# Kernel optimization log

Hardware: AMD Instinct MI355X
Metric: run time of the kernel (lower is better)

Reference implementation:

```python
import jax, jax.numpy as jnp
import numpy as np

TOP_K = 5
THRESHOLD = 0.0
EPS = 1e-12

def l2_normalize(x, axis):
    sq = jnp.sum(x * x, axis=axis, keepdims=True)
    return x * jax.lax.rsqrt(jnp.maximum(sq, EPS))

def setup_inputs() -> dict:
    key = jax.random.key(0)
    k1, k2, k3, k4 = jax.random.split(key, 4)
    B, S, D = 256, 197, 768
    P, L, T = 20, 5, 10
    x_embed = jax.random.normal(k1, (B, S, D), dtype=jnp.float32)
    prompt = jax.random.uniform(k2, (P, L, D), dtype=jnp.float32, minval=-1.0, maxval=1.0)
    prompt_key = jax.random.uniform(k3, (P, D), dtype=jnp.float32, minval=-1.0, maxval=1.0)
    assist_prompt = jax.random.uniform(k4, (T, L, D), dtype=jnp.float32, minval=-1.0, maxval=1.0)
    return {"x_embed": x_embed, "prompt": prompt, "prompt_key": prompt_key,
            "assist_prompt": assist_prompt, "test": 0}

def reference(x_embed, prompt, prompt_key, assist_prompt, test):
    B = x_embed.shape[0]
    D = x_embed.shape[-1]
    # embedding key: mean over tokens
    x_mean = jnp.mean(x_embed, axis=1)                 # [B, D]
    x_norm = l2_normalize(x_mean, axis=1)              # [B, D]  (test >= 0 branch)
    p_norm = l2_normalize(prompt_key, axis=1)          # [P, D]
    similarity = x_norm @ p_norm.T                     # [B, P]
    vals, idx = jax.lax.top_k(similarity, TOP_K)       # sorted descending -> pruning mask is a prefix
    keep = vals > THRESHOLD                            # [B, K]
    idx_pruned = jnp.where(keep, idx, -1)              # [B, K], -1 = dummy prompt
    idx_safe = jnp.maximum(idx_pruned, 0)
    # gather selected prompts, zero-out pruned slots (dummy prompts)
    sel = jnp.where(keep[:, :, None, None], prompt[idx_safe], 0.0)     # [B, K, L, D]
    assist_b = jnp.broadcast_to(assist_prompt, (B,) + assist_prompt.shape)  # [B, T, L, D]
    selected = jnp.concatenate([assist_b, sel], axis=1)                # [B, T+K, L, D]
    tokens = selected.reshape(B, -1, D)                                # [B, (T+K)*L, D]
    # reduce_sim: sum over all valid (b,k) keys of key . x_b', summed over b', / B
    gathered_keys = jnp.where(keep[:, :, None], p_norm[idx_safe], 0.0) # [B, K, D]
    key_total = jnp.sum(gathered_keys, axis=(0, 1))                    # [D]
    reduce_sim = jnp.dot(jnp.sum(x_norm, axis=0), key_total) / B
    prompted_embedding = jnp.concatenate([tokens, x_embed], axis=1)    # [B, (T+K)*L + S, D]
    return prompted_embedding, reduce_sim, tokens, idx_pruned, x_norm
```

## Files before the change

kernel.cpp:

```cpp
#include <hip/hip_runtime.h>

#define B 256
#define S 197
#define D 768
#define P 20
#define L 5
#define T 10
#define K 5

#define ROWS_PE 272
#define SZ_PE   (B * ROWS_PE * D)
#define OFF_RS  ((long)SZ_PE)
#define OFF_TOK (OFF_RS + 1)
#define SZ_TOK  (B * (T + K) * L * D)
#define OFF_IDX (OFF_TOK + SZ_TOK)
#define OFF_XN  (OFF_IDX + B * K)

typedef float f4 __attribute__((ext_vector_type(4)));

__global__ void __launch_bounds__(192)
k_mean_copy(const float* __restrict__ x, float* __restrict__ pe,
            float* __restrict__ partial) {
    const int tile = blockIdx.x & 3;
    const int b = blockIdx.x >> 2;
    const int t = threadIdx.x;
    const int s0 = tile * 50;
    const int s1 = (s0 + 50 < S) ? s0 + 50 : S;
    const f4* x4 = (const f4*)x;
    f4* o4 = (f4*)pe;
    const int xbase = b * S * (D / 4) + t;
    const int obase = (b * ROWS_PE + (T + K) * L) * (D / 4) + t;
    f4 acc = {0.f, 0.f, 0.f, 0.f};
    for (int s = s0; s < s1; ++s) {
        f4 v = __builtin_nontemporal_load(x4 + xbase + s * (D / 4));
        acc += v;
        __builtin_nontemporal_store(v, o4 + obase + s * (D / 4));
    }
    ((f4*)partial)[blockIdx.x * (D / 4) + t] = acc;
}

__global__ void __launch_bounds__(256)
k_fuse(const float* __restrict__ partial, const float* __restrict__ pkey,
       const float* __restrict__ prompt, const float* __restrict__ assist,
       float* __restrict__ pe, float* __restrict__ tok,
       float* __restrict__ xnorm_out, float* __restrict__ idxp_f,
       float* __restrict__ xsum, int* __restrict__ keycnt,
       unsigned int* __restrict__ done, float* __restrict__ rs) {
    const int t = threadIdx.x;

    if (blockIdx.x >= B) {
        const int item = (blockIdx.x - B) * 256 + t;
        const int b = item / 9600;
        const int r = item - b * 9600;
        const int j = r / 192;
        const int c = r - j * 192;
        const f4 v = ((const f4*)assist)[j * 192 + c];
        __builtin_nontemporal_store(v, (f4*)pe + ((long)b * ROWS_PE + j) * 192 + c);
        float* d2 = tok + ((long)b * 75 + j) * 768 + 4 * c;
        __builtin_nontemporal_store(v[0], d2 + 0);
        __builtin_nontemporal_store(v[1], d2 + 1);
        __builtin_nontemporal_store(v[2], d2 + 2);
        __builtin_nontemporal_store(v[3], d2 + 3);
        return;
    }

    const int b = blockIdx.x;
    const int lane = t & 63, wid = t >> 6;
    __shared__ float xs[D];
    __shared__ float sim[P];
    __shared__ float red[4];
    __shared__ float coef[P];
    __shared__ int sidx[K];
    __shared__ int amLast;

    float v0 = 0.f, v1 = 0.f, v2 = 0.f;
    for (int tile = 0; tile < 4; ++tile) {
        const float* pp = partial + (b * 4 + tile) * D;
        v0 += pp[t]; v1 += pp[t + 256]; v2 += pp[t + 512];
    }
    const float invS = 1.0f / (float)S;
    v0 *= invS; v1 *= invS; v2 *= invS;
    float ss = v0 * v0 + v1 * v1 + v2 * v2;
    for (int o = 32; o > 0; o >>= 1) ss += __shfl_down(ss, o);
    if (lane == 0) red[wid] = ss;
    __syncthreads();
    if (t == 0) red[0] = rsqrtf(fmaxf(red[0] + red[1] + red[2] + red[3], 1e-12f));
    __syncthreads();
    const float rn = red[0];
    v0 *= rn; v1 *= rn; v2 *= rn;
    xs[t] = v0; xs[t + 256] = v1; xs[t + 512] = v2;
    xnorm_out[b * D + t] = v0;
    xnorm_out[b * D + t + 256] = v1;
    xnorm_out[b * D + t + 512] = v2;
    atomicAdd(&xsum[t], v0);
    atomicAdd(&xsum[t + 256], v1);
    atomicAdd(&xsum[t + 512], v2);
    __syncthreads();

    for (int p = wid; p < P; p += 4) {
        const float* pr = pkey + p * D;
        float axk = 0.f, akk = 0.f;
        for (int d = lane; d < D; d += 64) {
            const float kv = pr[d];
            axk += xs[d] * kv;
            akk += kv * kv;
        }
        for (int o = 32; o > 0; o >>= 1) {
            axk += __shfl_down(axk, o);
            akk += __shfl_down(akk, o);
        }
        if (lane == 0) sim[p] = axk * rsqrtf(fmaxf(akk, 1e-12f));
    }
    __syncthreads();

    if (t == 0) {
        unsigned usedMask = 0u;
        for (int k = 0; k < K; ++k) {
            float best = -INFINITY; int bi = 0;
            for (int p = 0; p < P; ++p)
                if (!((usedMask >> p) & 1u) && sim[p] > best) { best = sim[p]; bi = p; }
            usedMask |= 1u << bi;
            const int oi = (best > 0.0f) ? bi : -1;
            sidx[k] = oi;
            idxp_f[b * K + k] = (float)oi;
            if (oi >= 0) atomicAdd(&keycnt[bi], 1);
        }
    }
    __syncthreads();

    for (int it = t; it < K * L * 192; it += 256) {
        const int j = it / 192;
        const int c = it - j * 192;
        const int k = j / L;
        const int l = j - k * L;
        const int idx = sidx[k];
        f4 v = {0.f, 0.f, 0.f, 0.f};
        if (idx >= 0) v = ((const f4*)prompt)[(idx * L + l) * 192 + c];
        __builtin_nontemporal_store(v, (f4*)pe + ((long)b * ROWS_PE + T * L + j) * 192 + c);
        float* d2 = tok + ((long)b * 75 + T * L + j) * 768 + 4 * c;
        __builtin_nontemporal_store(v[0], d2 + 0);
        __builtin_nontemporal_store(v[1], d2 + 1);
        __builtin_nontemporal_store(v[2], d2 + 2);
        __builtin_nontemporal_store(v[3], d2 + 3);
    }

    if (t == 0) {
        __threadfence();
        const unsigned prev =
            __hip_atomic_fetch_add(done, 1u, __ATOMIC_ACQ_REL, __HIP_MEMORY_SCOPE_AGENT);
        amLast = (prev == (unsigned)(B - 1)) ? 1 : 0;
    }
    __syncthreads();
    if (amLast) {
        for (int p = wid; p < P; p += 4) {
            const float* pr = pkey + p * D;
            float akk = 0.f;
            for (int d = lane; d < D; d += 64) { const float kv = pr[d]; akk += kv * kv; }
            for (int o = 32; o > 0; o >>= 1) akk += __shfl_down(akk, o);
            if (lane == 0) {
                const int cnt =
                    __hip_atomic_load(&keycnt[p], __ATOMIC_RELAXED, __HIP_MEMORY_SCOPE_AGENT);
                coef[p] = (float)cnt * rsqrtf(fmaxf(akk, 1e-12f));
            }
        }
        __syncthreads();
        float acc = 0.f;
        for (int cc = 0; cc < 3; ++cc) {
            const int d = t + cc * 256;
            float kt = 0.f;
            for (int p = 0; p < P; ++p) kt += coef[p] * pkey[p * D + d];
            const float xv =
                __hip_atomic_load(&xsum[d], __ATOMIC_RELAXED, __HIP_MEMORY_SCOPE_AGENT);
            acc += xv * kt;
        }
        for (int o = 32; o > 0; o >>= 1) acc += __shfl_down(acc, o);
        if (lane == 0) red[wid] = acc;
        __syncthreads();
        if (t == 0) rs[0] = (red[0] + red[1] + red[2] + red[3]) * (1.0f / (float)B);
    }
}

extern "C" void kernel_launch(void* const* d_in, const int* in_sizes, int n_in,
                              void* d_out, int out_size, void* d_ws, size_t ws_size,
                              hipStream_t stream) {
    const float* x      = (const float*)d_in[0];
    const float* prompt = (const float*)d_in[1];
    const float* pkey   = (const float*)d_in[2];
    const float* assist = (const float*)d_in[3];
    float* out = (float*)d_out;
    float* ws  = (float*)d_ws;

    float* partial   = ws;
    int*   keycnt    = (int*)(partial + B * 4 * D);
    float* xsum      = (float*)(keycnt + P);
    unsigned* done   = (unsigned*)(xsum + D);

    hipMemsetAsync(keycnt, 0, (P + D + 1) * sizeof(float), stream);

    k_mean_copy<<<dim3(4 * B), 192, 0, stream>>>(x, out, partial);
    k_fuse<<<dim3(B + 9600), 256, 0, stream>>>(partial, pkey, prompt, assist,
                                               out, out + OFF_TOK,
                                               out + OFF_XN, out + OFF_IDX,
                                               xsum, keycnt, done, out + OFF_RS);
}
```

Baseline: 449.8 us.

## Fuse mean-copy and per-batch fuse kernels via last-tile-arrives election

Merges the two kernels into one launch. Each of the four sequence tiles per batch row atomically increments a per-row counter after writing its partial sum, and the last tile to arrive does the normalize, similarity, top-k and prompt gather for that row. The goal is to drop one kernel launch and the grid-wide barrier between the streaming copy and the per-row work, so the gathers can overlap with ongoing copying. In exchange, the copy blocks now run with 256 threads while only 192 do work, and it adds atomic counter traffic.

```diff
diff --git a/kernel.cpp b/kernel.cpp
--- a/kernel.cpp
+++ b/kernel.cpp
@@ -16,40 +16,24 @@
 #define OFF_IDX (OFF_TOK + SZ_TOK)
 #define OFF_XN  (OFF_IDX + B * K)
 
+#define NPROD   (4 * B)
+#define NASSIST 9600
+
 typedef float f4 __attribute__((ext_vector_type(4)));
 
-__global__ void __launch_bounds__(192)
-k_mean_copy(const float* __restrict__ x, float* __restrict__ pe,
-            float* __restrict__ partial) {
-    const int tile = blockIdx.x & 3;
-    const int b = blockIdx.x >> 2;
+__global__ void __launch_bounds__(256)
+k_all(const float* __restrict__ x, const float* __restrict__ prompt,
+      const float* __restrict__ pkey, const float* __restrict__ assist,
+      float* __restrict__ pe, float* __restrict__ tok,
+      float* __restrict__ xnorm_out, float* __restrict__ idxp_f,
+      float* __restrict__ partial, float* __restrict__ xsum,
+      int* __restrict__ keycnt, unsigned* __restrict__ tile_done,
+      unsigned* __restrict__ done, float* __restrict__ rs) {
     const int t = threadIdx.x;
-    const int s0 = tile * 50;
-    const int s1 = (s0 + 50 < S) ? s0 + 50 : S;
-    const f4* x4 = (const f4*)x;
-    f4* o4 = (f4*)pe;
-    const int xbase = b * S * (D / 4) + t;
-    const int obase = (b * ROWS_PE + (T + K) * L) * (D / 4) + t;
-    f4 acc = {0.f, 0.f, 0.f, 0.f};
-    for (int s = s0; s < s1; ++s) {
-        f4 v = __builtin_nontemporal_load(x4 + xbase + s * (D / 4));
-        acc += v;
-        __builtin_nontemporal_store(v, o4 + obase + s * (D / 4));
-    }
-    ((f4*)partial)[blockIdx.x * (D / 4) + t] = acc;
-}
-
-__global__ void __launch_bounds__(256)
-k_fuse(const float* __restrict__ partial, const float* __restrict__ pkey,
-       const float* __restrict__ prompt, const float* __restrict__ assist,
-       float* __restrict__ pe, float* __restrict__ tok,
-       float* __restrict__ xnorm_out, float* __restrict__ idxp_f,
-       float* __restrict__ xsum, int* __restrict__ keycnt,
-       unsigned int* __restrict__ done, float* __restrict__ rs) {
-    const int t = threadIdx.x;
-
-    if (blockIdx.x >= B) {
-        const int item = (blockIdx.x - B) * 256 + t;
+    const int blk = blockIdx.x;
+
+    if (blk >= NPROD) {
+        const int item = (blk - NPROD) * 256 + t;
         const int b = item / 9600;
         const int r = item - b * 9600;
         const int j = r / 192;
@@ -64,7 +48,35 @@
         return;
     }
 
-    const int b = blockIdx.x;
+    const int b = blk >> 2;
+    const int tile = blk & 3;
+    if (t < 192) {
+        const int s0 = tile * 50;
+        const int s1 = (s0 + 50 < S) ? s0 + 50 : S;
+        const f4* x4 = (const f4*)x;
+        f4* o4 = (f4*)pe;
+        const int xbase = b * S * 192 + t;
+        const int obase = (b * ROWS_PE + (T + K) * L) * 192 + t;
+        f4 acc = {0.f, 0.f, 0.f, 0.f};
+        for (int s = s0; s < s1; ++s) {
+            f4 v = __builtin_nontemporal_load(x4 + xbase + s * 192);
+            acc += v;
+            __builtin_nontemporal_store(v, o4 + obase + s * 192);
+        }
+        ((f4*)partial)[blk * 192 + t] = acc;
+    }
+
+    __shared__ int winner;
+    __syncthreads();
+    if (t == 0) {
+        __threadfence();
+        const unsigned prev = __hip_atomic_fetch_add(
+            &tile_done[b], 1u, __ATOMIC_ACQ_REL, __HIP_MEMORY_SCOPE_AGENT);
+        winner = (prev == 3u) ? 1 : 0;
+    }
+    __syncthreads();
+    if (!winner) return;
+
     const int lane = t & 63, wid = t >> 6;
     __shared__ float xs[D];
     __shared__ float sim[P];
@@ -74,9 +86,11 @@
     __shared__ int amLast;
 
     float v0 = 0.f, v1 = 0.f, v2 = 0.f;
-    for (int tile = 0; tile < 4; ++tile) {
-        const float* pp = partial + (b * 4 + tile) * D;
-        v0 += pp[t]; v1 += pp[t + 256]; v2 += pp[t + 512];
+    for (int tl = 0; tl < 4; ++tl) {
+        float* pp = partial + (b * 4 + tl) * D;
+        v0 += __hip_atomic_load(pp + t,       __ATOMIC_RELAXED, __HIP_MEMORY_SCOPE_AGENT);
+        v1 += __hip_atomic_load(pp + t + 256, __ATOMIC_RELAXED, __HIP_MEMORY_SCOPE_AGENT);
+        v2 += __hip_atomic_load(pp + t + 512, __ATOMIC_RELAXED, __HIP_MEMORY_SCOPE_AGENT);
     }
     const float invS = 1.0f / (float)S;
     v0 *= invS; v1 *= invS; v2 *= invS;
@@ -190,16 +204,15 @@
     float* out = (float*)d_out;
     float* ws  = (float*)d_ws;
 
-    float* partial   = ws;
-    int*   keycnt    = (int*)(partial + B * 4 * D);
-    float* xsum      = (float*)(keycnt + P);
-    unsigned* done   = (unsigned*)(xsum + D);
-
-    hipMemsetAsync(keycnt, 0, (P + D + 1) * sizeof(float), stream);
-
-    k_mean_copy<<<dim3(4 * B), 192, 0, stream>>>(x, out, partial);
-    k_fuse<<<dim3(B + 9600), 256, 0, stream>>>(partial, pkey, prompt, assist,
-                                               out, out + OFF_TOK,
-                                               out + OFF_XN, out + OFF_IDX,
-                                               xsum, keycnt, done, out + OFF_RS);
+    float*    partial   = ws;
+    int*      keycnt    = (int*)(partial + 4 * B * D);
+    float*    xsum      = (float*)(keycnt + P);
+    unsigned* done      = (unsigned*)(xsum + D);
+    unsigned* tile_done = done + 1;
+
+    hipMemsetAsync(keycnt, 0, (P + D + 1 + B) * sizeof(float), stream);
+
+    k_all<<<dim3(NPROD + NASSIST), 256, 0, stream>>>(
+        x, prompt, pkey, assist, out, out + OFF_TOK, out + OFF_XN, out + OFF_IDX,
+        partial, xsum, keycnt, tile_done, done, out + OFF_RS);
 }
```

Result: slower. 514.5 us (+14.4%).

## Fold memset into stream kernel, double threads per tile, vectorize token stores

Applied to the files above, without the earlier changes.

Removes the separate hipMemsetAsync by adding an extra block to the streaming kernel that zeroes the counters. The streaming kernel now uses 384 threads, with two halves interleaving rows and combining partial sums through LDS, to raise memory-level parallelism. Scalar nontemporal stores to the token output are replaced by a single 4-wide store with a 4-byte-aligned vector type. The in-kernel zeroing depends on the next kernel being stream-ordered after this one, which holds.

```diff
diff --git a/kernel.cpp b/kernel.cpp
--- a/kernel.cpp
+++ b/kernel.cpp
@@ -16,27 +16,41 @@
 #define OFF_IDX (OFF_TOK + SZ_TOK)
 #define OFF_XN  (OFF_IDX + B * K)
 
-typedef float f4 __attribute__((ext_vector_type(4)));
-
-__global__ void __launch_bounds__(192)
-k_mean_copy(const float* __restrict__ x, float* __restrict__ pe,
-            float* __restrict__ partial) {
-    const int tile = blockIdx.x & 3;
-    const int b = blockIdx.x >> 2;
+typedef float f4  __attribute__((ext_vector_type(4)));
+typedef float f4u __attribute__((ext_vector_type(4), aligned(4)));
+
+__global__ void __launch_bounds__(384)
+k_stream(const float* __restrict__ x, float* __restrict__ pe,
+         float* __restrict__ partial, unsigned* __restrict__ zstate) {
     const int t = threadIdx.x;
+    const int blk = blockIdx.x;
+    if (blk == 4 * B) {
+        for (int i = t; i < P + D + 1; i += 384) zstate[i] = 0u;
+        return;
+    }
+    const int b = blk >> 2;
+    const int tile = blk & 3;
+    const int half = (t >= 192) ? 1 : 0;
+    const int c = t - half * 192;
     const int s0 = tile * 50;
     const int s1 = (s0 + 50 < S) ? s0 + 50 : S;
     const f4* x4 = (const f4*)x;
     f4* o4 = (f4*)pe;
-    const int xbase = b * S * (D / 4) + t;
-    const int obase = (b * ROWS_PE + (T + K) * L) * (D / 4) + t;
+    const int xbase = b * S * 192 + c;
+    const int obase = (b * ROWS_PE + (T + K) * L) * 192 + c;
     f4 acc = {0.f, 0.f, 0.f, 0.f};
-    for (int s = s0; s < s1; ++s) {
-        f4 v = __builtin_nontemporal_load(x4 + xbase + s * (D / 4));
+    for (int s = s0 + half; s < s1; s += 2) {
+        f4 v = __builtin_nontemporal_load(x4 + xbase + s * 192);
         acc += v;
-        __builtin_nontemporal_store(v, o4 + obase + s * (D / 4));
-    }
-    ((f4*)partial)[blockIdx.x * (D / 4) + t] = acc;
+        __builtin_nontemporal_store(v, o4 + obase + s * 192);
+    }
+    __shared__ f4 lds[192];
+    if (half) lds[c] = acc;
+    __syncthreads();
+    if (!half) {
+        acc += lds[c];
+        ((f4*)partial)[blk * 192 + c] = acc;
+    }
 }
 
 __global__ void __launch_bounds__(256)
@@ -57,10 +71,8 @@
         const f4 v = ((const f4*)assist)[j * 192 + c];
         __builtin_nontemporal_store(v, (f4*)pe + ((long)b * ROWS_PE + j) * 192 + c);
         float* d2 = tok + ((long)b * 75 + j) * 768 + 4 * c;
-        __builtin_nontemporal_store(v[0], d2 + 0);
-        __builtin_nontemporal_store(v[1], d2 + 1);
-        __builtin_nontemporal_store(v[2], d2 + 2);
-        __builtin_nontemporal_store(v[3], d2 + 3);
+        f4u vu = v;
+        __builtin_nontemporal_store(vu, (f4u*)d2);
         return;
     }
 
@@ -138,10 +150,8 @@
         if (idx >= 0) v = ((const f4*)prompt)[(idx * L + l) * 192 + c];
         __builtin_nontemporal_store(v, (f4*)pe + ((long)b * ROWS_PE + T * L + j) * 192 + c);
         float* d2 = tok + ((long)b * 75 + T * L + j) * 768 + 4 * c;
-        __builtin_nontemporal_store(v[0], d2 + 0);
-        __builtin_nontemporal_store(v[1], d2 + 1);
-        __builtin_nontemporal_store(v[2], d2 + 2);
-        __builtin_nontemporal_store(v[3], d2 + 3);
+        f4u vu = v;
+        __builtin_nontemporal_store(vu, (f4u*)d2);
     }
 
     if (t == 0) {
@@ -190,14 +200,12 @@
     float* out = (float*)d_out;
     float* ws  = (float*)d_ws;
 
-    float* partial   = ws;
-    int*   keycnt    = (int*)(partial + B * 4 * D);
-    float* xsum      = (float*)(keycnt + P);
-    unsigned* done   = (unsigned*)(xsum + D);
-
-    hipMemsetAsync(keycnt, 0, (P + D + 1) * sizeof(float), stream);
-
-    k_mean_copy<<<dim3(4 * B), 192, 0, stream>>>(x, out, partial);
+    float*    partial = ws;
+    int*      keycnt  = (int*)(partial + 4 * B * D);
+    float*    xsum    = (float*)(keycnt + P);
+    unsigned* done    = (unsigned*)(xsum + D);
+
+    k_stream<<<dim3(4 * B + 1), 384, 0, stream>>>(x, out, partial, (unsigned*)keycnt);
     k_fuse<<<dim3(B + 9600), 256, 0, stream>>>(partial, pkey, prompt, assist,
                                                out, out + OFF_TOK,
                                                out + OFF_XN, out + OFF_IDX,
```

New measurement: 443.5 us. About the same (-1.4%).
